# Kernel optimization log

Measured on AMD Instinct MI355X. Metric: run time of the kernel, lower is better.

Reference implementation:

```python
import jax, jax.numpy as jnp
import numpy as np

TEMPERATURE = 8.0  # sqrt(d_k), d_k = 64
MINIMUM_VALUE = -1e9  # stand-in for C.MINIMUM_VALUE


def setup_inputs() -> dict:
    key = jax.random.key(0)
    kq, kk, kv, km = jax.random.split(key, 4)
    B, N, D = 32, 2048, 64
    q = jax.random.normal(kq, (B, N, D), dtype=jnp.float32)
    k = jax.random.normal(kk, (B, N, D), dtype=jnp.float32)
    v = jax.random.normal(kv, (B, N, D), dtype=jnp.float32)
    mask = jax.random.randint(km, (B, N, N), 0, 2, dtype=jnp.int32)
    return {"q": q, "k": k, "v": v, "mask": mask}


def reference(q, k, v, mask):
    # scores: [B, Nq, Nk]
    attn = jnp.einsum("bqd,bkd->bqk", q, k) / TEMPERATURE
    attn = jnp.where(mask > 0, attn, MINIMUM_VALUE)
    attn = jax.nn.softmax(attn, axis=-1)
    # dropout is identity in eval / deterministic reference
    output = jnp.einsum("bqk,bkd->bqd", attn, v)
    return (output, attn)
```

## Files before the change

### kernel.cpp

```cpp
#include <hip/hip_runtime.h>

#define NB 32
#define NN 2048
#define ND 64
#define ROWS 16
#define NBLK (NB * NN / ROWS)

#define LDS_PART 65536
#define LDS_TOTAL 66048

typedef _Float16 half8 __attribute__((ext_vector_type(8)));
typedef float f32x4 __attribute__((ext_vector_type(4)));
typedef int i32x4 __attribute__((ext_vector_type(4)));

union H4 { uint2 u; _Float16 h[4]; };
union H8 { uint4 u; _Float16 h[8]; };

__device__ __forceinline__ f32x4 mfma16(half8 a, half8 b, f32x4 c) {
    return __builtin_amdgcn_mfma_f32_16x16x32_f16(a, b, c, 0, 0, 0);
}
#define SB() __builtin_amdgcn_sched_barrier(0)

__global__ __launch_bounds__(256) void cvt_f32_f16_k(const float* __restrict__ src,
                                                     _Float16* __restrict__ dst) {
    int i = blockIdx.x * 256 + threadIdx.x;
    const f32x4* s = (const f32x4*)src;
    f32x4 a = s[2 * i], b = s[2 * i + 1];
    half8 h;
    h[0] = (_Float16)a[0]; h[1] = (_Float16)a[1]; h[2] = (_Float16)a[2]; h[3] = (_Float16)a[3];
    h[4] = (_Float16)b[0]; h[5] = (_Float16)b[1]; h[6] = (_Float16)b[2]; h[7] = (_Float16)b[3];
    ((half8*)dst)[i] = h;
}

__global__ __launch_bounds__(256) void transpose_v_k(const float* __restrict__ v,
                                                     _Float16* __restrict__ vt) {
    __shared__ float tile[64][65];
    int b = blockIdx.x >> 5;
    int k0 = (blockIdx.x & 31) * 64;
    int t = threadIdx.x;
    {
        int dc = t & 15, kr = t >> 4;
        const f32x4* vp = (const f32x4*)(v + ((size_t)(b * NN + k0) * ND));
        #pragma unroll
        for (int i = 0; i < 4; ++i) {
            int kk = kr + i * 16;
            f32x4 x = vp[kk * 16 + dc];
            tile[kk][dc * 4 + 0] = x[0]; tile[kk][dc * 4 + 1] = x[1];
            tile[kk][dc * 4 + 2] = x[2]; tile[kk][dc * 4 + 3] = x[3];
        }
    }
    __syncthreads();
    {
        int d = t >> 2, ks = (t & 3) * 16;
        union { _Float16 hh[16]; uint4 u4[2]; } pk;
        #pragma unroll
        for (int j = 0; j < 16; ++j) pk.hh[j] = (_Float16)tile[ks + j][d];
        uint4* op = (uint4*)(vt + ((size_t)(b * ND + d) * NN + k0 + ks));
        op[0] = pk.u4[0]; op[1] = pk.u4[1];
    }
}

__global__ __launch_bounds__(256) void mask_pack_k(const int* __restrict__ mask,
                                                   unsigned long long* __restrict__ pm) {
    size_t gid = (size_t)blockIdx.x * 256 + threadIdx.x;
    size_t row = gid >> 5;
    int w = ((int)gid >> 2) & 7, lg = (int)gid & 3;
    const i32x4* mp = (const i32x4*)(mask + row * NN + w * 16 + lg * 4);
    unsigned long long bits = 0ull;
    #pragma unroll
    for (int i = 0; i < 16; i += 4) {
        i32x4 m0 = __builtin_nontemporal_load(mp + (size_t)(i + 0) * 32);
        i32x4 m1 = __builtin_nontemporal_load(mp + (size_t)(i + 1) * 32);
        i32x4 m2 = __builtin_nontemporal_load(mp + (size_t)(i + 2) * 32);
        i32x4 m3 = __builtin_nontemporal_load(mp + (size_t)(i + 3) * 32);
        unsigned b0 = (m0[0] > 0 ? 1u : 0u) | (m0[1] > 0 ? 2u : 0u) | (m0[2] > 0 ? 4u : 0u) | (m0[3] > 0 ? 8u : 0u);
        unsigned b1 = (m1[0] > 0 ? 1u : 0u) | (m1[1] > 0 ? 2u : 0u) | (m1[2] > 0 ? 4u : 0u) | (m1[3] > 0 ? 8u : 0u);
        unsigned b2 = (m2[0] > 0 ? 1u : 0u) | (m2[1] > 0 ? 2u : 0u) | (m2[2] > 0 ? 4u : 0u) | (m2[3] > 0 ? 8u : 0u);
        unsigned b3 = (m3[0] > 0 ? 1u : 0u) | (m3[1] > 0 ? 2u : 0u) | (m3[2] > 0 ? 4u : 0u) | (m3[3] > 0 ? 8u : 0u);
        bits |= (unsigned long long)(b0 | (b1 << 4) | (b2 << 8) | (b3 << 12)) << (i * 4);
    }
    pm[gid] = bits;
}

#define LDK(S, base) { \
    const _Float16* kk_ = kp + (size_t)(base) * (128 * ND); \
    S##0a = *(const half8*)(kk_);                S##0b = *(const half8*)(kk_ + 32); \
    S##1a = *(const half8*)(kk_ + 128 * ND);     S##1b = *(const half8*)(kk_ + 128 * ND + 32); \
    S##2a = *(const half8*)(kk_ + 2 * 128 * ND); S##2b = *(const half8*)(kk_ + 2 * 128 * ND + 32); \
    S##3a = *(const half8*)(kk_ + 3 * 128 * ND); S##3b = *(const half8*)(kk_ + 3 * 128 * ND + 32); }

#define CMP1(i, ka_, kb_) { \
    f32x4 acc = {0.f, 0.f, 0.f, 0.f}; \
    acc = mfma16(ka_, qf0, acc); \
    acc = mfma16(kb_, qf1, acc); \
    unsigned mb = (unsigned)(pmask >> ((i) * 4)) & 15u; \
    float e0 = (mb & 1u) ? __expf(acc[0] * 0.125f) : 0.f; \
    float e1 = (mb & 2u) ? __expf(acc[1] * 0.125f) : 0.f; \
    float e2 = (mb & 4u) ? __expf(acc[2] * 0.125f) : 0.f; \
    float e3 = (mb & 8u) ? __expf(acc[3] * 0.125f) : 0.f; \
    rsum += (e0 + e1) + (e2 + e3); \
    H4 y_; y_.h[0] = (_Float16)e0; y_.h[1] = (_Float16)e1; \
    y_.h[2] = (_Float16)e2; y_.h[3] = (_Float16)e3; \
    *(uint2*)(srow + ((((w * 16 + (i) * 128) + lg * 4) * 2) ^ sw)) = y_.u; }

#define CMP4(S, c) { CMP1((c)*4 + 0, S##0a, S##0b) CMP1((c)*4 + 1, S##1a, S##1b) \
                     CMP1((c)*4 + 2, S##2a, S##2b) CMP1((c)*4 + 3, S##3a, S##3b) }

#define LDV(S, base) { \
    const _Float16* vv_ = vp + (size_t)(base) * 32; \
    S##0 = *(const half8*)(vv_);       S##1 = *(const half8*)(vv_ + 32); \
    S##2 = *(const half8*)(vv_ + 64);  S##3 = *(const half8*)(vv_ + 96); \
    S##4 = *(const half8*)(vv_ + 128); S##5 = *(const half8*)(vv_ + 160); \
    S##6 = *(const half8*)(vv_ + 192); S##7 = *(const half8*)(vv_ + 224); }

#define PV1(ks_, vb_) { \
    half8 pa_ = *(const half8*)(pbase + ((((ks_) * 64) + lg * 16) ^ sw)); \
    o = mfma16(pa_, vb_, o); }

#define PV8(S, base) { PV1((base) + 0, S##0) PV1((base) + 1, S##1) \
                       PV1((base) + 2, S##2) PV1((base) + 3, S##3) \
                       PV1((base) + 4, S##4) PV1((base) + 5, S##5) \
                       PV1((base) + 6, S##6) PV1((base) + 7, S##7) }

#define NRM(jj) { \
    int colb_ = g * 16 + (jj) * 256; \
    H8 x_; x_.u = *(const uint4*)(s2 + (colb_ ^ sw2)); \
    f32x4 a0_, a1_; \
    a0_[0] = (float)x_.h[0] * linv; a0_[1] = (float)x_.h[1] * linv; \
    a0_[2] = (float)x_.h[2] * linv; a0_[3] = (float)x_.h[3] * linv; \
    a1_[0] = (float)x_.h[4] * linv; a1_[1] = (float)x_.h[5] * linv; \
    a1_[2] = (float)x_.h[6] * linv; a1_[3] = (float)x_.h[7] * linv; \
    __builtin_nontemporal_store(a0_, (f32x4*)(arow + (colb_ >> 1))); \
    __builtin_nontemporal_store(a1_, (f32x4*)(arow + (colb_ >> 1) + 4)); }

__global__ __launch_bounds__(512, 4) void attn_main_k(
        const _Float16* __restrict__ qh, const _Float16* __restrict__ kh,
        const _Float16* __restrict__ vtp, const unsigned long long* __restrict__ pm,
        float* __restrict__ outp, float* __restrict__ attnp) {
    extern __shared__ char smem[];

    int bid = blockIdx.x;
    int lin = (bid & 7) * (NBLK / 8) + (bid >> 3);
    int b  = lin >> 7;
    int q0 = (lin & 127) * ROWS;

    int t = threadIdx.x;
    int w = t >> 6, l = t & 63;
    int l15 = l & 15, lg = l >> 4;
    int sw = (l15 & 7) << 4;

    const _Float16* qb = qh + ((size_t)(b * NN + q0 + l15) * ND) + lg * 8;
    half8 qf0 = *(const half8*)(qb);
    half8 qf1 = *(const half8*)(qb + 32);

    unsigned long long pmask = pm[((size_t)(b * NN + q0 + l15) * 8 + w) * 4 + lg];

    const _Float16* kp = kh + (size_t)b * NN * ND + (size_t)(w * 16 + l15) * ND + lg * 8;
    char* srow = smem + l15 * 4096;

    half8 A0a, A0b, A1a, A1b, A2a, A2b, A3a, A3b;
    half8 B0a, B0b, B1a, B1b, B2a, B2b, B3a, B3b;
    float rsum = 0.f;
    LDK(A, 0)  SB();
    LDK(B, 4)  SB();
    CMP4(A, 0) SB();
    LDK(A, 8)  SB();
    CMP4(B, 1) SB();
    LDK(B, 12) SB();
    CMP4(A, 2) SB();
    CMP4(B, 3)

    rsum += __shfl_xor(rsum, 16);
    rsum += __shfl_xor(rsum, 32);
    float* part = (float*)(smem + LDS_PART);
    if (l < 16) part[w * 16 + l] = rsum;
    __syncthreads();

    if (w < 4) {
        const _Float16* vp = vtp + (size_t)(b * ND + w * 16 + l15) * NN + lg * 8;
        char* pbase = smem + l15 * 4096;
        f32x4 o = {0.f, 0.f, 0.f, 0.f};
        half8 V0, V1, V2, V3, V4, V5, V6, V7;
        half8 W0, W1, W2, W3, W4, W5, W6, W7;
        LDV(V, 0)   SB();
        LDV(W, 8)   SB();
        PV8(V, 0)   SB();
        LDV(V, 16)  SB();
        PV8(W, 8)   SB();
        LDV(W, 24)  SB();
        PV8(V, 16)  SB();
        LDV(V, 32)  SB();
        PV8(W, 24)  SB();
        LDV(W, 40)  SB();
        PV8(V, 32)  SB();
        LDV(V, 48)  SB();
        PV8(W, 40)  SB();
        LDV(W, 56)  SB();
        PV8(V, 48)  SB();
        PV8(W, 56)

        float* ob = outp + ((size_t)(b * NN + q0 + lg * 4)) * ND + w * 16 + l15;
        #pragma unroll
        for (int rr = 0; rr < 4; ++rr) {
            int qr = lg * 4 + rr;
            float s8 = 0.f;
            #pragma unroll
            for (int pw = 0; pw < 8; ++pw) s8 += part[pw * 16 + qr];
            __builtin_nontemporal_store(o[rr] / (s8 + 1e-37f), ob + (size_t)rr * ND);
        }
    } else {
        int r = (w - 4) * 4 + lg;
        int g = l15;
        float su = 0.f;
        #pragma unroll
        for (int pw = 0; pw < 8; ++pw) su += part[pw * 16 + r];
        float linv = 1.0f / (su + 1e-37f);
        char* s2 = smem + r * 4096;
        int sw2 = (r & 7) << 4;
        float* arow = attnp + ((size_t)(b * NN + q0 + r)) * NN;
        NRM(0)  NRM(1)  NRM(2)  NRM(3)
        NRM(4)  NRM(5)  NRM(6)  NRM(7)
        NRM(8)  NRM(9)  NRM(10) NRM(11)
        NRM(12) NRM(13) NRM(14) NRM(15)
    }
}

extern "C" void kernel_launch(void* const* d_in, const int* in_sizes, int n_in,
                              void* d_out, int out_size, void* d_ws, size_t ws_size,
                              hipStream_t stream) {
    const float* q = (const float*)d_in[0];
    const float* k = (const float*)d_in[1];
    const float* v = (const float*)d_in[2];
    const int* mask = (const int*)d_in[3];
    float* outp  = (float*)d_out;
    float* attnp = outp + (size_t)NB * NN * ND;

    _Float16* qh = (_Float16*)d_ws;
    _Float16* kh = qh + (size_t)NB * NN * ND;
    _Float16* vth = kh + (size_t)NB * NN * ND;
    unsigned long long* pm = (unsigned long long*)(vth + (size_t)NB * NN * ND);

    cvt_f32_f16_k<<<2048, 256, 0, stream>>>(q, qh);
    cvt_f32_f16_k<<<2048, 256, 0, stream>>>(k, kh);
    transpose_v_k<<<1024, 256, 0, stream>>>(v, vth);
    mask_pack_k<<<8192, 256, 0, stream>>>(mask, pm);
    attn_main_k<<<NBLK, 512, LDS_TOTAL, stream>>>(qh, kh, vth, pm, outp, attnp);
}
```

Before: 418.3 us.

## Make attention kernel persistent with per-block loop over eight row tiles

```diff
diff --git a/kernel.cpp b/kernel.cpp
--- a/kernel.cpp
+++ b/kernel.cpp
@@ -4,7 +4,8 @@
 #define NN 2048
 #define ND 64
 #define ROWS 16
-#define NBLK (NB * NN / ROWS)
+#define NTILE (NB * NN / ROWS)
+#define NBLK 512
 
 #define LDS_PART 65536
 #define LDS_TOTAL 66048
@@ -14,12 +15,14 @@
 typedef int i32x4 __attribute__((ext_vector_type(4)));
 
 union H4 { uint2 u; _Float16 h[4]; };
-union H8 { uint4 u; _Float16 h[8]; };
 
 __device__ __forceinline__ f32x4 mfma16(half8 a, half8 b, f32x4 c) {
     return __builtin_amdgcn_mfma_f32_16x16x32_f16(a, b, c, 0, 0, 0);
 }
 #define SB() __builtin_amdgcn_sched_barrier(0)
+#define LBAR() { asm volatile("s_waitcnt lgkmcnt(0)" ::: "memory"); \
+                 __builtin_amdgcn_s_barrier(); \
+                 __builtin_amdgcn_sched_barrier(0); }
 
 __global__ __launch_bounds__(256) void cvt_f32_f16_k(const float* __restrict__ src,
                                                      _Float16* __restrict__ dst) {
@@ -123,15 +126,12 @@
                        PV1((base) + 6, S##6) PV1((base) + 7, S##7) }
 
 #define NRM(jj) { \
-    int colb_ = g * 16 + (jj) * 256; \
-    H8 x_; x_.u = *(const uint4*)(s2 + (colb_ ^ sw2)); \
-    f32x4 a0_, a1_; \
-    a0_[0] = (float)x_.h[0] * linv; a0_[1] = (float)x_.h[1] * linv; \
-    a0_[2] = (float)x_.h[2] * linv; a0_[3] = (float)x_.h[3] * linv; \
-    a1_[0] = (float)x_.h[4] * linv; a1_[1] = (float)x_.h[5] * linv; \
-    a1_[2] = (float)x_.h[6] * linv; a1_[3] = (float)x_.h[7] * linv; \
-    __builtin_nontemporal_store(a0_, (f32x4*)(arow + (colb_ >> 1))); \
-    __builtin_nontemporal_store(a1_, (f32x4*)(arow + (colb_ >> 1) + 4)); }
+    int colb_ = (l15 * 8 + (jj) * 128); \
+    H4 x_; x_.u = *(const uint2*)(s2 + (colb_ ^ sw2)); \
+    f32x4 av_; \
+    av_[0] = (float)x_.h[0] * linv; av_[1] = (float)x_.h[1] * linv; \
+    av_[2] = (float)x_.h[2] * linv; av_[3] = (float)x_.h[3] * linv; \
+    __builtin_nontemporal_store(av_, (f32x4*)(arow + (colb_ >> 1))); }
 
 __global__ __launch_bounds__(512, 4) void attn_main_k(
         const _Float16* __restrict__ qh, const _Float16* __restrict__ kh,
@@ -139,89 +139,95 @@
         float* __restrict__ outp, float* __restrict__ attnp) {
     extern __shared__ char smem[];
 
-    int bid = blockIdx.x;
-    int lin = (bid & 7) * (NBLK / 8) + (bid >> 3);
-    int b  = lin >> 7;
-    int q0 = (lin & 127) * ROWS;
+    int p = blockIdx.x;
+    int xcd = p & 7, slot = p >> 3;
 
     int t = threadIdx.x;
     int w = t >> 6, l = t & 63;
     int l15 = l & 15, lg = l >> 4;
     int sw = (l15 & 7) << 4;
-
-    const _Float16* qb = qh + ((size_t)(b * NN + q0 + l15) * ND) + lg * 8;
-    half8 qf0 = *(const half8*)(qb);
-    half8 qf1 = *(const half8*)(qb + 32);
-
-    unsigned long long pmask = pm[((size_t)(b * NN + q0 + l15) * 8 + w) * 4 + lg];
-
-    const _Float16* kp = kh + (size_t)b * NN * ND + (size_t)(w * 16 + l15) * ND + lg * 8;
     char* srow = smem + l15 * 4096;
-
-    half8 A0a, A0b, A1a, A1b, A2a, A2b, A3a, A3b;
-    half8 B0a, B0b, B1a, B1b, B2a, B2b, B3a, B3b;
-    float rsum = 0.f;
-    LDK(A, 0)  SB();
-    LDK(B, 4)  SB();
-    CMP4(A, 0) SB();
-    LDK(A, 8)  SB();
-    CMP4(B, 1) SB();
-    LDK(B, 12) SB();
-    CMP4(A, 2) SB();
-    CMP4(B, 3)
-
-    rsum += __shfl_xor(rsum, 16);
-    rsum += __shfl_xor(rsum, 32);
     float* part = (float*)(smem + LDS_PART);
-    if (l < 16) part[w * 16 + l] = rsum;
-    __syncthreads();
-
-    if (w < 4) {
-        const _Float16* vp = vtp + (size_t)(b * ND + w * 16 + l15) * NN + lg * 8;
-        char* pbase = smem + l15 * 4096;
-        f32x4 o = {0.f, 0.f, 0.f, 0.f};
-        half8 V0, V1, V2, V3, V4, V5, V6, V7;
-        half8 W0, W1, W2, W3, W4, W5, W6, W7;
-        LDV(V, 0)   SB();
-        LDV(W, 8)   SB();
-        PV8(V, 0)   SB();
-        LDV(V, 16)  SB();
-        PV8(W, 8)   SB();
-        LDV(W, 24)  SB();
-        PV8(V, 16)  SB();
-        LDV(V, 32)  SB();
-        PV8(W, 24)  SB();
-        LDV(W, 40)  SB();
-        PV8(V, 32)  SB();
-        LDV(V, 48)  SB();
-        PV8(W, 40)  SB();
-        LDV(W, 56)  SB();
-        PV8(V, 48)  SB();
-        PV8(W, 56)
-
-        float* ob = outp + ((size_t)(b * NN + q0 + lg * 4)) * ND + w * 16 + l15;
-        #pragma unroll
-        for (int rr = 0; rr < 4; ++rr) {
-            int qr = lg * 4 + rr;
-            float s8 = 0.f;
+
+    for (int it = 0; it < 8; ++it) {
+        int lin = xcd * (NTILE / 8) + slot * 8 + it;
+        int b  = lin >> 7;
+        int q0 = (lin & 127) * ROWS;
+
+        const _Float16* qb = qh + ((size_t)(b * NN + q0 + l15) * ND) + lg * 8;
+        half8 qf0 = *(const half8*)(qb);
+        half8 qf1 = *(const half8*)(qb + 32);
+        unsigned long long pmask = pm[((size_t)(b * NN + q0 + l15) * 8 + w) * 4 + lg];
+        const _Float16* kp = kh + (size_t)b * NN * ND + (size_t)(w * 16 + l15) * ND + lg * 8;
+
+        half8 A0a, A0b, A1a, A1b, A2a, A2b, A3a, A3b;
+        half8 B0a, B0b, B1a, B1b, B2a, B2b, B3a, B3b;
+        float rsum = 0.f;
+        LDK(A, 0)  SB();
+        LDK(B, 4)  SB();
+        CMP4(A, 0) SB();
+        LDK(A, 8)  SB();
+        CMP4(B, 1) SB();
+        LDK(B, 12) SB();
+        CMP4(A, 2) SB();
+        CMP4(B, 3)
+
+        rsum += __shfl_xor(rsum, 16);
+        rsum += __shfl_xor(rsum, 32);
+        if (l < 16) part[w * 16 + l] = rsum;
+        LBAR();
+
+        if (w < 4) {
+            const _Float16* vp = vtp + (size_t)(b * ND + w * 16 + l15) * NN + lg * 8;
+            char* pbase = smem + l15 * 4096;
+            f32x4 o = {0.f, 0.f, 0.f, 0.f};
+            half8 V0, V1, V2, V3, V4, V5, V6, V7;
+            half8 W0, W1, W2, W3, W4, W5, W6, W7;
+            LDV(V, 0)   SB();
+            LDV(W, 8)   SB();
+            PV8(V, 0)   SB();
+            LDV(V, 16)  SB();
+            PV8(W, 8)   SB();
+            LDV(W, 24)  SB();
+            PV8(V, 16)  SB();
+            LDV(V, 32)  SB();
+            PV8(W, 24)  SB();
+            LDV(W, 40)  SB();
+            PV8(V, 32)  SB();
+            LDV(V, 48)  SB();
+            PV8(W, 40)  SB();
+            LDV(W, 56)  SB();
+            PV8(V, 48)  SB();
+            PV8(W, 56)
+
+            float* ob = outp + ((size_t)(b * NN + q0 + lg * 4)) * ND + w * 16 + l15;
             #pragma unroll
-            for (int pw = 0; pw < 8; ++pw) s8 += part[pw * 16 + qr];
-            __builtin_nontemporal_store(o[rr] / (s8 + 1e-37f), ob + (size_t)rr * ND);
+            for (int rr = 0; rr < 4; ++rr) {
+                int qr = lg * 4 + rr;
+                float s8 = 0.f;
+                #pragma unroll
+                for (int pw = 0; pw < 8; ++pw) s8 += part[pw * 16 + qr];
+                __builtin_nontemporal_store(o[rr] / (s8 + 1e-37f), ob + (size_t)rr * ND);
+            }
+        } else {
+            int r = (w - 4) * 4 + lg;
+            float su = 0.f;
+            #pragma unroll
+            for (int pw = 0; pw < 8; ++pw) su += part[pw * 16 + r];
+            float linv = 1.0f / (su + 1e-37f);
+            char* s2 = smem + r * 4096;
+            int sw2 = (r & 7) << 4;
+            float* arow = attnp + ((size_t)(b * NN + q0 + r)) * NN;
+            NRM(0)  NRM(1)  NRM(2)  NRM(3)
+            NRM(4)  NRM(5)  NRM(6)  NRM(7)
+            NRM(8)  NRM(9)  NRM(10) NRM(11)
+            NRM(12) NRM(13) NRM(14) NRM(15)
+            NRM(16) NRM(17) NRM(18) NRM(19)
+            NRM(20) NRM(21) NRM(22) NRM(23)
+            NRM(24) NRM(25) NRM(26) NRM(27)
+            NRM(28) NRM(29) NRM(30) NRM(31)
         }
-    } else {
-        int r = (w - 4) * 4 + lg;
-        int g = l15;
-        float su = 0.f;
-        #pragma unroll
-        for (int pw = 0; pw < 8; ++pw) su += part[pw * 16 + r];
-        float linv = 1.0f / (su + 1e-37f);
-        char* s2 = smem + r * 4096;
-        int sw2 = (r & 7) << 4;
-        float* arow = attnp + ((size_t)(b * NN + q0 + r)) * NN;
-        NRM(0)  NRM(1)  NRM(2)  NRM(3)
-        NRM(4)  NRM(5)  NRM(6)  NRM(7)
-        NRM(8)  NRM(9)  NRM(10) NRM(11)
-        NRM(12) NRM(13) NRM(14) NRM(15)
+        LBAR();
     }
 }
 
```

New measurement: 716.1 us. 71.2% more time.
